# Optimization experiments

Hardware: AMD Instinct MI355X
Metric: run time of the kernel (lower is better)

Reference implementation:

```python
import jax, jax.numpy as jnp
import numpy as np

B, P, M, N, H, K, EH = 16, 50, 512, 1024, 64, 20, 200


def setup_inputs() -> dict:
    key = jax.random.key(0)
    ks = jax.random.split(key, 16)
    b = jax.random.normal(ks[0], (B, P, M, 1), jnp.float32)
    A = jax.random.normal(ks[1], (1, P, M, N), jnp.float32) / np.float32(np.sqrt(M))
    # random undirected multigraph on P nodes, stored with both directions
    s = jax.random.randint(ks[2], (B, EH), 0, P)
    off = jax.random.randint(ks[3], (B, EH), 1, P)
    d = (s + off) % P
    edge_index = jnp.stack([jnp.concatenate([s, d], 1), jnp.concatenate([d, s], 1)], 1).astype(jnp.int32)  # [B,2,2*EH]

    def lin(k, fi, fo, scale=None):
        scale = np.float32(1.0 / np.sqrt(fi)) if scale is None else np.float32(scale)
        return jax.random.normal(k, (fi, fo), jnp.float32) * scale, jnp.zeros((fo,), jnp.float32)

    W_e1, b_e1 = lin(ks[4], P * M, P * H)
    W_e2, b_e2 = lin(ks[5], P * H, 2 * P * H)
    W_e3, b_e3 = lin(ks[6], 2 * P * H, 4 * P * H)
    W_c1, b_c1 = lin(ks[7], 4 * H, 2 * H)
    W_c2, b_c2 = lin(ks[8], 2 * H, 2 * H)
    W_f1, b_f1 = lin(ks[9], 2 * H, H)
    W_f2, _ = lin(ks[10], H, K * 4, scale=1e-3)
    b_f2 = jnp.full((K * 4,), -2.0, jnp.float32)  # mimics fc2 init (tiny weights, negative bias)
    max_param = jnp.array([0.01, 0.1, 0.1, 0.1], jnp.float32).reshape(1, 1, 1, 4)  # [alpha,tau,rho,eta]_max
    y0 = jax.random.normal(ks[11], (B, P, N, 1), jnp.float32) * 0.01
    u0 = jax.random.normal(ks[12], (B, P, N, 1), jnp.float32) * 0.01
    d0 = jax.random.normal(ks[13], (B, P, N, 1), jnp.float32) * 0.01
    return dict(b=b, A=A, edge_index=edge_index, max_param=max_param,
                W_e1=W_e1, b_e1=b_e1, W_e2=W_e2, b_e2=b_e2, W_e3=W_e3, b_e3=b_e3,
                W_c1=W_c1, b_c1=b_c1, W_c2=W_c2, b_c2=b_c2,
                W_f1=W_f1, b_f1=b_f1, W_f2=W_f2, b_f2=b_f2,
                y0=y0, u0=u0, d0=d0)


def _lrelu(x):
    return jax.nn.leaky_relu(x, 0.01)


def _gcn(x, s, d, W, bias):
    # GCNConv: sym-normalized propagation with self loops. x: [P,F]
    h = x @ W
    deg = jnp.zeros((x.shape[0],), x.dtype).at[d].add(1.0) + 1.0  # +1 self loop
    dinv = jax.lax.rsqrt(deg)
    agg = jnp.zeros_like(h).at[d].add(h[s] * (dinv[s] * dinv[d])[:, None])
    agg = agg + h * (dinv * dinv)[:, None]  # self-loop term
    return agg + bias


def _delta(y, s, d):
    # nested neighbor loop: for each directed edge (s,d): delta[s]+=y[s]-y[d]; delta[d]-=same
    diff = y[s] - y[d]  # [E,N,1]
    return jnp.zeros_like(y).at[s].add(diff).at[d].add(-diff)


def reference(b, A, edge_index, max_param,
              W_e1, b_e1, W_e2, b_e2, W_e3, b_e3,
              W_c1, b_c1, W_c2, b_c2, W_f1, b_f1, W_f2, b_f2,
              y0, u0, d0):
    Bb = b.shape[0]
    n = A.shape[3]
    k_steps = W_f2.shape[1] // 4
    src, dst = edge_index[:, 0], edge_index[:, 1]

    # ---- GNN hypernetwork ----
    x = b.reshape(Bb, -1)
    x = _lrelu(x @ W_e1 + b_e1)
    x = _lrelu(x @ W_e2 + b_e2)
    x = (x @ W_e3 + b_e3).reshape(Bb, P, -1)  # [B,P,4H]
    x = _lrelu(jax.vmap(lambda xf, s, d: _gcn(xf, s, d, W_c1, b_c1))(x, src, dst))
    x = _lrelu(jax.vmap(lambda xf, s, d: _gcn(xf, s, d, W_c2, b_c2))(x, src, dst))
    x = x.mean(axis=1)  # global_mean_pool over nodes
    x = _lrelu(x @ W_f1 + b_f1)
    hyp = (x @ W_f2 + b_f2).reshape(Bb, k_steps, 1, 4)
    hyp = jax.nn.sigmoid(jnp.cumsum(hyp, axis=1)) * max_param  # [B,K,1,4]
    hyp_scan = jnp.transpose(hyp, (1, 3, 0, 2))[..., None, None]  # [K,4,B,1,1,1]

    # ---- precompute ----
    A0 = A[0]  # [P,M,N]
    AtA = jnp.einsum('pmn,pmk->pnk', A0, A0)  # [P,N,N]
    Atb = jnp.einsum('pmn,bpmo->bpno', A0, b)  # [B,P,N,1]
    sum_nb = jax.vmap(lambda s: jnp.zeros((P,), b.dtype).at[s].add(1.0))(src)[:, :, None, None]  # [B,P,1,1]

    # ---- unrolled D-ADMM / DLASSO ----
    def step(carry, hk):
        y_k, U_k, dlt = carry
        alpha, tau, rho, eta = hk[0], hk[1], hk[2], hk[3]
        AtAy = jnp.einsum('pnk,bpko->bpno', AtA, y_k)
        g = AtAy - Atb + jnp.sign(y_k) * tau + U_k * sum_nb + dlt * rho
        y_n = y_k - alpha * g
        dlt_n = jax.vmap(_delta)(y_n, src, dst)
        U_n = U_k + dlt_n * eta
        return (y_n, U_n, dlt_n), y_n

    _, Y = jax.lax.scan(step, (y0, u0, d0), hyp_scan)
    return Y  # [K,B,P,N,1]
```

## Files before the change

### kernel.cpp

```cpp
#include <hip/hip_runtime.h>

namespace {
constexpr int NB = 16;
constexpr int NP = 50;
constexpr int NM = 512;
constexpr int NN = 1024;
constexpr int NK = 20;
constexpr long ASZ = (long)NP * NM * NN;
constexpr long YSZ = (long)NB * NP * NN;
}

typedef __attribute__((ext_vector_type(8))) short bf16x8;
typedef __attribute__((ext_vector_type(4))) float f32x4;

__device__ __forceinline__ float lrelu(float x){ return x > 0.f ? x : 0.01f*x; }
__device__ __forceinline__ float bfu(unsigned short x){
  unsigned v = ((unsigned)x) << 16;
  return __builtin_bit_cast(float, v);
}
__device__ __forceinline__ unsigned short f2bf(float f){
  unsigned u = __builtin_bit_cast(unsigned, f);
  u += 0x7fffu + ((u >> 16) & 1u);
  return (unsigned short)(u >> 16);
}

__global__ __launch_bounds__(256) void k_prep(const float* __restrict__ A,
                      unsigned short* __restrict__ abfT){
  const int p = blockIdx.x, mt = blockIdx.y, nt = blockIdx.z;
  const int tid = threadIdx.x;
  __shared__ unsigned short tile[64][72];
  const int m0 = mt*64, n0 = nt*64;
  {
    int r = tid>>2, cs = (tid&3)*16;
    const float* src = A + ((long)p*NM + m0 + r)*NN + n0 + cs;
    unsigned short tmp[16];
    #pragma unroll
    for (int q=0;q<16;q+=4){
      float4 v = *(const float4*)(src+q);
      tmp[q+0]=f2bf(v.x); tmp[q+1]=f2bf(v.y); tmp[q+2]=f2bf(v.z); tmp[q+3]=f2bf(v.w);
    }
    #pragma unroll
    for (int q=0;q<16;q++) tile[r][cs+q] = tmp[q];
  }
  __syncthreads();
  {
    int r = tid>>2, cs = (tid&3)*16;
    unsigned short* dst = abfT + ((long)p*NN + n0 + r)*NM + m0 + cs;
    unsigned short tmp[16];
    #pragma unroll
    for (int q=0;q<16;q++) tmp[q] = tile[cs+q][r];
    #pragma unroll
    for (int q=0;q<16;q+=8) *(uint4*)(dst+q) = *(const uint4*)&tmp[q];
  }
}

__global__ void k_init(const float* __restrict__ y0, const float* __restrict__ u0,
                       float* __restrict__ y, float* __restrict__ u,
                       unsigned short* __restrict__ ybf, int n){
  int e = (blockIdx.x*blockDim.x + threadIdx.x)*4;
  if (e >= n) return;
  float4 a = *(const float4*)(y0+e);
  *(float4*)(y+e) = a;
  ushort4 o; o.x=f2bf(a.x); o.y=f2bf(a.y); o.z=f2bf(a.z); o.w=f2bf(a.w);
  *(ushort4*)(ybf+e) = o;
  *(float4*)(u+e)  = *(const float4*)(u0+e);
}

__global__ __launch_bounds__(256) void k_c0(const float* __restrict__ u0,
      const float* __restrict__ d0, const float* __restrict__ snbg,
      const float* __restrict__ hypg, float* __restrict__ c){
  long e = ((long)blockIdx.x*256 + threadIdx.x)*4;
  if (e >= YSZ) return;
  long bp = e >> 10;
  int b = (int)(bp/NP), p = (int)(bp%NP);
  float sp = snbg[b*NP+p], rho = hypg[b*80 + 2];
  float4 uv = *(const float4*)(u0+e);
  float4 dv = *(const float4*)(d0+e);
  float4 cv;
  cv.x = uv.x*sp + dv.x*rho; cv.y = uv.y*sp + dv.y*rho;
  cv.z = uv.z*sp + dv.z*rho; cv.w = uv.w*sp + dv.w*rho;
  *(float4*)(c+e) = cv;
}

__global__ __launch_bounds__(256) void k_atb(const unsigned short* __restrict__ abfT,
                      const float* __restrict__ src, float* __restrict__ z){
  const int p = blockIdx.x;
  const int tid = threadIdx.x, wave = tid>>6, lane = tid&63;
  __shared__ unsigned short tlds[16][520];
  {
    int b = tid>>4, c0 = (tid&15)*8;
    const float* tr = src + ((long)b*NP + p)*NM;
    #pragma unroll
    for (int it=0; it<4; it++){
      float4 lo = *(const float4*)(tr + it*128 + c0);
      float4 hi = *(const float4*)(tr + it*128 + c0 + 4);
      unsigned short w[8];
      w[0]=f2bf(lo.x); w[1]=f2bf(lo.y); w[2]=f2bf(lo.z); w[3]=f2bf(lo.w);
      w[4]=f2bf(hi.x); w[5]=f2bf(hi.y); w[6]=f2bf(hi.z); w[7]=f2bf(hi.w);
      *(uint4*)&tlds[b][it*128 + c0] = *(const uint4*)w;
    }
  }
  __syncthreads();
  const int lr = lane&15, kg = lane>>4;
  const int nt0 = blockIdx.y*4 + wave;
  const int n0 = nt0*16, n1 = (nt0+32)*16;
  const unsigned short* b0 = abfT + ((long)p*NN + n0 + lr)*NM + kg*8;
  const unsigned short* b1 = abfT + ((long)p*NN + n1 + lr)*NM + kg*8;
  const unsigned short* tp = &tlds[lr][kg*8];
  f32x4 acc0a={0.f,0.f,0.f,0.f}, acc0b={0.f,0.f,0.f,0.f};
  f32x4 acc1a={0.f,0.f,0.f,0.f}, acc1b={0.f,0.f,0.f,0.f};
  #pragma unroll 4
  for (int ks=0; ks<16; ks+=2){
    bf16x8 t0 = *(const bf16x8*)(tp + ks*32);
    bf16x8 t1 = *(const bf16x8*)(tp + ks*32 + 32);
    bf16x8 b00 = *(const bf16x8*)(b0 + (long)ks*32);
    bf16x8 b01 = *(const bf16x8*)(b0 + (long)ks*32 + 32);
    bf16x8 b10 = *(const bf16x8*)(b1 + (long)ks*32);
    bf16x8 b11 = *(const bf16x8*)(b1 + (long)ks*32 + 32);
    acc0a = __builtin_amdgcn_mfma_f32_16x16x32_bf16(t0, b00, acc0a, 0, 0, 0);
    acc1a = __builtin_amdgcn_mfma_f32_16x16x32_bf16(t0, b10, acc1a, 0, 0, 0);
    acc0b = __builtin_amdgcn_mfma_f32_16x16x32_bf16(t1, b01, acc0b, 0, 0, 0);
    acc1b = __builtin_amdgcn_mfma_f32_16x16x32_bf16(t1, b11, acc1b, 0, 0, 0);
  }
  f32x4 acc0 = acc0a + acc0b;
  f32x4 acc1 = acc1a + acc1b;
  #pragma unroll
  for (int r=0;r<4;r++){
    int bb = kg*4 + r;
    z[((long)bb*NP + p)*NN + n0 + lr] = acc0[r];
    z[((long)bb*NP + p)*NN + n1 + lr] = acc1[r];
  }
}

__global__ __launch_bounds__(256) void k_ata(const unsigned short* __restrict__ abfT,
                      unsigned short* __restrict__ ata){
  const int p = blockIdx.y;
  int yy = blockIdx.x, bi = 0;
  while (yy >= 8 - bi){ yy -= 8 - bi; bi++; }
  const int bj = bi + yy;
  const int i0 = bi*128, j0 = bj*128;
  const int tid = threadIdx.x, wave = tid>>6, lane = tid&63;
  const int lr = lane&15, kg = lane>>4;
  __shared__ unsigned short pa[128][72];
  __shared__ unsigned short pb[128][72];
  f32x4 acc[2][8];
  #pragma unroll
  for (int ti=0;ti<2;ti++)
    #pragma unroll
    for (int tj=0;tj<8;tj++) acc[ti][tj] = (f32x4){0.f,0.f,0.f,0.f};
  const unsigned short* Abase = abfT + (long)p*NN*NM;
  for (int mc=0; mc<NM; mc+=64){
    __syncthreads();
    {
      int r = tid>>1, c0 = (tid&1)*32;
      const unsigned short* sa = Abase + (long)(i0 + r)*NM + mc + c0;
      const unsigned short* sb = Abase + (long)(j0 + r)*NM + mc + c0;
      #pragma unroll
      for (int q=0;q<32;q+=8){
        *(uint4*)&pa[r][c0+q] = *(const uint4*)(sa+q);
        *(uint4*)&pb[r][c0+q] = *(const uint4*)(sb+q);
      }
    }
    __syncthreads();
    #pragma unroll
    for (int ks=0; ks<2; ks++){
      bf16x8 av0 = *(const bf16x8*)&pa[wave*32      + lr][ks*32 + kg*8];
      bf16x8 av1 = *(const bf16x8*)&pa[wave*32 + 16 + lr][ks*32 + kg*8];
      #pragma unroll
      for (int tj=0;tj<8;tj++){
        bf16x8 bv = *(const bf16x8*)&pb[tj*16 + lr][ks*32 + kg*8];
        acc[0][tj] = __builtin_amdgcn_mfma_f32_16x16x32_bf16(av0, bv, acc[0][tj], 0,0,0);
        acc[1][tj] = __builtin_amdgcn_mfma_f32_16x16x32_bf16(av1, bv, acc[1][tj], 0,0,0);
      }
    }
  }
  const long pbase = (long)p << 20;
  #pragma unroll
  for (int ti=0; ti<2; ti++){
    const int ib = i0 + wave*32 + ti*16;
    #pragma unroll
    for (int tj=0; tj<8; tj++){
      const int jb = j0 + tj*16;
      unsigned short w[4];
      #pragma unroll
      for (int r=0;r<4;r++) w[r] = f2bf(acc[ti][tj][r]);
      #pragma unroll
      for (int r=0;r<4;r++)
        ata[pbase + (long)(ib + kg*4 + r)*1024 + jb + lr] = w[r];
      if (bi != bj)
        *(ushort4*)(ata + pbase + (long)(jb + lr)*1024 + ib + kg*4) = *(const ushort4*)w;
    }
  }
}

__global__ __launch_bounds__(256) void k_enc2(const float* __restrict__ X, const float* __restrict__ W,
                           float* __restrict__ part, int fi, int fo, int ichunk, int actin){
  const int tid = threadIdx.x;
  const int o0 = (blockIdx.x*256 + tid)*4;
  const int c  = blockIdx.y;
  const bool ok = o0 < fo;
  __shared__ float xs[64][16];
  float4 acc[16];
  #pragma unroll
  for (int b=0;b<16;b++){ acc[b].x=0.f; acc[b].y=0.f; acc[b].z=0.f; acc[b].w=0.f; }
  const long ibase = (long)c*ichunk;
  const int xb = tid&15, xio = (tid>>4)*4;
  for (int s=0; s<ichunk; s+=64){
    float4 v = *(const float4*)(X + (long)xb*fi + ibase + s + xio);
    if (actin){ v.x=lrelu(v.x); v.y=lrelu(v.y); v.z=lrelu(v.z); v.w=lrelu(v.w); }
    __syncthreads();
    xs[xio+0][xb]=v.x; xs[xio+1][xb]=v.y; xs[xio+2][xb]=v.z; xs[xio+3][xb]=v.w;
    __syncthreads();
    const float* wp = W + (ibase+s)*fo + o0;
    #pragma unroll 4
    for (int i=0;i<64;i++){
      float4 w;
      if (ok) w = *(const float4*)(wp + (long)i*fo);
      else { w.x=0.f; w.y=0.f; w.z=0.f; w.w=0.f; }
      #pragma unroll
      for (int b2=0;b2<16;b2+=4){
        float4 x4 = *(const float4*)&xs[i][b2];
        acc[b2+0].x += w.x*x4.x; acc[b2+0].y += w.y*x4.x; acc[b2+0].z += w.z*x4.x; acc[b2+0].w += w.w*x4.x;
        acc[b2+1].x += w.x*x4.y; acc[b2+1].y += w.y*x4.y; acc[b2+1].z += w.z*x4.y; acc[b2+1].w += w.w*x4.y;
        acc[b2+2].x += w.x*x4.z; acc[b2+2].y += w.y*x4.z; acc[b2+2].z += w.z*x4.z; acc[b2+2].w += w.w*x4.z;
        acc[b2+3].x += w.x*x4.w; acc[b2+3].y += w.y*x4.w; acc[b2+3].z += w.z*x4.w; acc[b2+3].w += w.w*x4.w;
      }
    }
  }
  if (ok){
    float* pp = part + ((long)c*16)*fo + o0;
    #pragma unroll
    for (int b=0;b<16;b++) *(float4*)(pp + (long)b*fo) = acc[b];
  }
}

__global__ void k_enc_reduce(const float* __restrict__ part, const float* __restrict__ bias,
                             float* __restrict__ out, int fo, int nchunk){
  int i = blockIdx.x*256 + threadIdx.x;
  if (i >= 16*fo) return;
  int o = i % fo;
  float s = bias[o];
  for (int c=0;c<nchunk;c++) s += part[(long)c*16*fo + i];
  out[i] = s;
}

__global__ __launch_bounds__(64) void k_graph(const int* __restrict__ ei, float* __restrict__ adjg,
                        float* __restrict__ dmg, float* __restrict__ snbg){
  const int b = blockIdx.x, tid = threadIdx.x;
  __shared__ float adj[2500], dm[2500], deg[50], dinv[50], snb[50];
  for (int i=tid;i<2500;i+=64){ adj[i]=0.f; dm[i]=0.f; }
  if (tid<50){ deg[tid]=0.f; snb[tid]=0.f; }
  __syncthreads();
  const int* e = ei + b*800;
  for (int k=tid;k<400;k+=64){
    atomicAdd(&deg[e[400+k]], 1.f);
    atomicAdd(&snb[e[k]], 1.f);
  }
  __syncthreads();
  if (tid<50) dinv[tid] = 1.f / sqrtf(deg[tid] + 1.f);
  __syncthreads();
  for (int k=tid;k<400;k+=64){
    int s = e[k], d = e[400+k];
    atomicAdd(&adj[d*50+s], dinv[s]*dinv[d]);
    atomicAdd(&dm[s*50+s],  1.f); atomicAdd(&dm[s*50+d], -1.f);
    atomicAdd(&dm[d*50+d],  1.f); atomicAdd(&dm[d*50+s], -1.f);
  }
  __syncthreads();
  if (tid<50) adj[tid*50+tid] += dinv[tid]*dinv[tid];
  __syncthreads();
  for (int i=tid;i<2500;i+=64){ adjg[b*2500+i]=adj[i]; dmg[b*2500+i]=dm[i]; }
  if (tid<50) snbg[b*50+tid]=snb[tid];
}

__global__ __launch_bounds__(256) void k_gnn(const float* __restrict__ h3,
     const float* __restrict__ Wc1, const float* __restrict__ bc1,
     const float* __restrict__ Wc2, const float* __restrict__ bc2,
     const float* __restrict__ Wf1, const float* __restrict__ bf1,
     const float* __restrict__ Wf2, const float* __restrict__ bf2,
     const float* __restrict__ maxp, const float* __restrict__ adjg,
     float* __restrict__ hypg){
  const int b = blockIdx.x, tid = threadIdx.x;
  __shared__ float adj[2500];
  __shared__ float bufA[6400];
  __shared__ float bufB[6400];
  __shared__ float xm[128], hv1[64], raw[80];
  for (int i=tid;i<2500;i+=256) adj[i] = adjg[b*2500+i];

  const int j = tid & 127, nh = tid >> 7;
  float acc[25];
  #pragma unroll
  for (int q=0;q<25;q++) acc[q]=0.f;
  for (int ic=0; ic<4; ic++){
    __syncthreads();
    for (int e=tid; e<800; e+=256){
      int n = e>>4, seg = (e&15)*4;
      *(float4*)&bufB[n*64+seg] = *(const float4*)(h3 + (long)b*12800 + n*256 + ic*64 + seg);
    }
    __syncthreads();
    for (int i=0;i<64;i+=4){
      float w0 = Wc1[(long)(ic*64+i+0)*128 + j];
      float w1 = Wc1[(long)(ic*64+i+1)*128 + j];
      float w2 = Wc1[(long)(ic*64+i+2)*128 + j];
      float w3 = Wc1[(long)(ic*64+i+3)*128 + j];
      #pragma unroll
      for (int q=0;q<25;q++){
        float4 xv = *(const float4*)&bufB[(nh*25+q)*64 + i];
        acc[q] += xv.x*w0 + xv.y*w1 + xv.z*w2 + xv.w*w3;
      }
    }
  }
  __syncthreads();
  #pragma unroll
  for (int q=0;q<25;q++) bufA[(nh*25+q)*128 + j] = acc[q];
  __syncthreads();
  {
    float a2[25];
    float bv = bc1[j];
    #pragma unroll
    for (int q=0;q<25;q++) a2[q]=bv;
    for (int qq=0; qq<50; qq++){
      float hvv = bufA[qq*128 + j];
      #pragma unroll
      for (int q=0;q<25;q++) a2[q] += adj[(nh*25+q)*50 + qq]*hvv;
    }
    __syncthreads();
    #pragma unroll
    for (int q=0;q<25;q++) bufB[(nh*25+q)*128 + j] = lrelu(a2[q]);
  }
  __syncthreads();
  {
    float a2[25];
    #pragma unroll
    for (int q=0;q<25;q++) a2[q]=0.f;
    for (int i=0;i<128;i+=4){
      float w0 = Wc2[(long)(i+0)*128 + j];
      float w1 = Wc2[(long)(i+1)*128 + j];
      float w2 = Wc2[(long)(i+2)*128 + j];
      float w3 = Wc2[(long)(i+3)*128 + j];
      #pragma unroll
      for (int q=0;q<25;q++){
        float4 xv = *(const float4*)&bufB[(nh*25+q)*128 + i];
        a2[q] += xv.x*w0 + xv.y*w1 + xv.z*w2 + xv.w*w3;
      }
    }
    __syncthreads();
    #pragma unroll
    for (int q=0;q<25;q++) bufA[(nh*25+q)*128 + j] = a2[q];
  }
  __syncthreads();
  {
    float a2[25];
    float bv = bc2[j];
    #pragma unroll
    for (int q=0;q<25;q++) a2[q]=bv;
    for (int qq=0; qq<50; qq++){
      float hvv = bufA[qq*128 + j];
      #pragma unroll
      for (int q=0;q<25;q++) a2[q] += adj[(nh*25+q)*50 + qq]*hvv;
    }
    __syncthreads();
    #pragma unroll
    for (int q=0;q<25;q++) bufB[(nh*25+q)*128 + j] = lrelu(a2[q]);
  }
  __syncthreads();
  if (tid < 128){
    float s = 0.f;
    for (int n=0;n<50;n++) s += bufB[n*128 + tid];
    xm[tid] = s * (1.f/50.f);
  }
  __syncthreads();
  if (tid < 64){
    float s = bf1[tid];
    for (int i=0;i<128;i++) s += xm[i]*Wf1[i*64 + tid];
    hv1[tid] = lrelu(s);
  }
  __syncthreads();
  if (tid < 80){
    float s = bf2[tid];
    for (int i=0;i<64;i++) s += hv1[i]*Wf2[i*80 + tid];
    raw[tid] = s;
  }
  __syncthreads();
  if (tid < 4){
    float c = 0.f;
    for (int k=0;k<20;k++){
      c += raw[k*4 + tid];
      hypg[b*80 + k*4 + tid] = maxp[tid] / (1.f + expf(-c));
    }
  }
}

__global__ __launch_bounds__(256, 4) void k_z(const unsigned short* __restrict__ ata,
      const unsigned short* __restrict__ ybin, const float* __restrict__ atb,
      const float* __restrict__ cbuf, const float* __restrict__ hypg, int k,
      float* __restrict__ y, unsigned short* __restrict__ ybout,
      float* __restrict__ yout){
  const int p = blockIdx.x;
  const int tid = threadIdx.x, wave = tid>>6, lane = tid&63;
  __shared__ unsigned short ylds[16][1032];
  {
    int b = tid>>4, c0 = (tid&15)*8;
    const unsigned short* yr = ybin + ((long)b*NP + p)*NN;
    #pragma unroll
    for (int it=0; it<8; it++)
      *(uint4*)&ylds[b][it*128 + c0] = *(const uint4*)(yr + it*128 + c0);
  }
  const int lr = lane&15, kg = lane>>4;
  const int n0 = (blockIdx.y*4 + wave)*16;
  const long pb2 = (long)p << 20;
  const unsigned short* bp = ata + pb2 + (long)(n0 + lr)*1024 + kg*8;
  const unsigned short* yp = &ylds[lr][kg*8];

  bf16x8 B[3][4];
  #pragma unroll
  for (int j=0;j<4;j++) B[0][j] = *(const bf16x8*)(bp + (0*4+j)*32);
  #pragma unroll
  for (int j=0;j<4;j++) B[1][j] = *(const bf16x8*)(bp + (1*4+j)*32);

  float yv4[4], atb4[4], c4[4];
  float4 hp4[4];
  #pragma unroll
  for (int r=0;r<4;r++){
    const int b = kg*4 + r;
    const long idx = ((long)b*NP + p)*NN + n0 + lr;
    yv4[r] = y[idx]; atb4[r] = atb[idx]; c4[r] = cbuf[idx];
    hp4[r] = *(const float4*)(hypg + b*80 + k*4);
  }
  __syncthreads();

  f32x4 a0={0.f,0.f,0.f,0.f}, a1={0.f,0.f,0.f,0.f}, a2={0.f,0.f,0.f,0.f}, a3={0.f,0.f,0.f,0.f};
  #pragma unroll
  for (int i=0;i<8;i++){
    const int cur = i % 3;
    const int nxt = (i+2) % 3;
    if (i < 6){
      #pragma unroll
      for (int j=0;j<4;j++) B[nxt][j] = *(const bf16x8*)(bp + ((i+2)*4+j)*32);
    }
    bf16x8 q0 = *(const bf16x8*)(yp + (i*4+0)*32);
    bf16x8 q1 = *(const bf16x8*)(yp + (i*4+1)*32);
    bf16x8 q2 = *(const bf16x8*)(yp + (i*4+2)*32);
    bf16x8 q3 = *(const bf16x8*)(yp + (i*4+3)*32);
    a0 = __builtin_amdgcn_mfma_f32_16x16x32_bf16(q0, B[cur][0], a0, 0,0,0);
    a1 = __builtin_amdgcn_mfma_f32_16x16x32_bf16(q1, B[cur][1], a1, 0,0,0);
    a2 = __builtin_amdgcn_mfma_f32_16x16x32_bf16(q2, B[cur][2], a2, 0,0,0);
    a3 = __builtin_amdgcn_mfma_f32_16x16x32_bf16(q3, B[cur][3], a3, 0,0,0);
  }
  f32x4 z = (a0 + a1) + (a2 + a3);
  #pragma unroll
  for (int r=0;r<4;r++){
    const int b = kg*4 + r;
    const long idx = ((long)b*NP + p)*NN + n0 + lr;
    float yv = yv4[r];
    float g = z[r] - atb4[r] + ((yv>0.f)?1.f:((yv<0.f)?-1.f:0.f))*hp4[r].y + c4[r];
    float ynv = yv - hp4[r].x*g;
    y[idx] = ynv; ybout[idx] = f2bf(ynv); yout[(long)k*YSZ + idx] = ynv;
  }
}

__global__ __launch_bounds__(256) void k_dm(const float* __restrict__ dmg,
      const float* __restrict__ snbg, const float* __restrict__ hypg, int k,
      const unsigned short* __restrict__ ybf, float* __restrict__ u, float* __restrict__ c){
  const int b = blockIdx.x, n0 = blockIdx.y*128, tid = threadIdx.x;
  __shared__ float ys[50][128];
  __shared__ float dms[2500];
  for (int i=tid;i<2500;i+=256) dms[i] = dmg[b*2500+i];
  for (int e=tid; e<6400; e+=256){
    int p=e>>7, nn=e&127;
    ys[p][nn] = bfu(ybf[((long)b*NP+p)*NN + n0 + nn]);
  }
  __syncthreads();
  const float eta = hypg[b*80 + k*4 + 3];
  const float rhon = hypg[b*80 + (k+1)*4 + 2];
  for (int e=tid; e<6400; e+=256){
    int p=e>>7, nn=e&127;
    float s=0.f;
    #pragma unroll 10
    for (int q=0;q<NP;q++) s += dms[p*50+q]*ys[q][nn];
    long idx = ((long)b*NP+p)*NN + n0 + nn;
    float un = u[idx] + s*eta;
    u[idx] = un;
    c[idx] = un*snbg[b*NP+p] + s*rhon;
  }
}

extern "C" void kernel_launch(void* const* d_in, const int* in_sizes, int n_in,
                              void* d_out, int out_size, void* d_ws, size_t ws_size,
                              hipStream_t stream){
  (void)in_sizes; (void)n_in; (void)out_size; (void)ws_size;
  const float* bin = (const float*)d_in[0];
  const float* A   = (const float*)d_in[1];
  const int*   ei  = (const int*)d_in[2];
  const float* mxp = (const float*)d_in[3];
  const float* We1 = (const float*)d_in[4];  const float* be1 = (const float*)d_in[5];
  const float* We2 = (const float*)d_in[6];  const float* be2 = (const float*)d_in[7];
  const float* We3 = (const float*)d_in[8];  const float* be3 = (const float*)d_in[9];
  const float* Wc1 = (const float*)d_in[10]; const float* bc1 = (const float*)d_in[11];
  const float* Wc2 = (const float*)d_in[12]; const float* bc2 = (const float*)d_in[13];
  const float* Wf1 = (const float*)d_in[14]; const float* bf1 = (const float*)d_in[15];
  const float* Wf2 = (const float*)d_in[16]; const float* bf2 = (const float*)d_in[17];
  const float* y0  = (const float*)d_in[18];
  const float* u0  = (const float*)d_in[19];
  const float* dd0 = (const float*)d_in[20];
  float* out = (float*)d_out;

  char* cur = (char*)d_ws;
  auto alloc = [&](size_t bytes)->void*{
    void* pp = (void*)cur; cur += (bytes + 255) & ~(size_t)255; return pp;
  };
  unsigned short* abfT = (unsigned short*)alloc(ASZ*2);
  unsigned short* ata  = (unsigned short*)alloc((size_t)NP*1024*1024*2);
  float* atb = (float*)alloc(YSZ*4);
  float* y   = (float*)alloc(YSZ*4);
  unsigned short* ybf0 = (unsigned short*)alloc(YSZ*2);
  unsigned short* ybf1 = (unsigned short*)alloc(YSZ*2);
  float* u   = (float*)alloc(YSZ*4);
  float* cb  = (float*)alloc(YSZ*4);
  float* h1  = (float*)alloc((size_t)16*3200*4);
  float* h2  = (float*)alloc((size_t)16*6400*4);
  float* h3  = (float*)alloc((size_t)16*12800*4);
  float* adj = (float*)alloc((size_t)16*2500*4);
  float* dm  = (float*)alloc((size_t)16*2500*4);
  float* snb = (float*)alloc((size_t)16*50*4);
  float* hyp = (float*)alloc((size_t)16*80*4);
  float* part= (float*)alloc((size_t)84000000);

  k_prep<<<dim3(50,8,16), dim3(256), 0, stream>>>(A, abfT);
  k_init<<<dim3(800), dim3(256), 0, stream>>>(y0, u0, y, u, ybf0, (int)YSZ);
  k_atb<<<dim3(50,8), dim3(256), 0, stream>>>(abfT, bin, atb);
  k_ata<<<dim3(36,50), dim3(256), 0, stream>>>(abfT, ata);

  k_enc2<<<dim3(4,200),  dim3(256), 0, stream>>>(bin, We1, part, 25600, 3200, 128, 0);
  k_enc_reduce<<<dim3(200), dim3(256), 0, stream>>>(part, be1, h1, 3200, 200);
  k_enc2<<<dim3(7,50),  dim3(256), 0, stream>>>(h1, We2, part, 3200, 6400, 64, 1);
  k_enc_reduce<<<dim3(400), dim3(256), 0, stream>>>(part, be2, h2, 6400, 50);
  k_enc2<<<dim3(13,100), dim3(256), 0, stream>>>(h2, We3, part, 6400, 12800, 64, 1);
  k_enc_reduce<<<dim3(800), dim3(256), 0, stream>>>(part, be3, h3, 12800, 100);

  k_graph<<<dim3(16), dim3(64), 0, stream>>>(ei, adj, dm, snb);
  k_gnn<<<dim3(16), dim3(256), 0, stream>>>(h3, Wc1, bc1, Wc2, bc2, Wf1, bf1, Wf2, bf2, mxp, adj, hyp);
  k_c0<<<dim3(800), dim3(256), 0, stream>>>(u0, dd0, snb, hyp, cb);

  for (int k=0;k<NK;k++){
    const unsigned short* ybin = (k & 1) ? ybf1 : ybf0;
    unsigned short* ybout      = (k & 1) ? ybf0 : ybf1;
    k_z<<<dim3(50,16), dim3(256), 0, stream>>>(ata, ybin, atb, cb, hyp, k, y, ybout, out);
    if (k < NK-1){
      const unsigned short* ybnew = (k & 1) ? ybf0 : ybf1;
      k_dm<<<dim3(16,8), dim3(256), 0, stream>>>(dm, snb, hyp, k, ybnew, u, cb);
    }
  }
}
```

Before: 1.532 ms.

## Tile AtA layout for contiguous MFMA loads and fold Atb into state buffer

Stores AtA in a 16x32 tiled layout so each wave's B-fragment loads in k_z read contiguous 512-element tiles instead of rows strided by 1024 elements. It also replaces the U state with w = U*sum_nb - Atb and precomputes e = w + rho*delta, so k_z reads one fp32 buffer per element instead of two. The tiled layout makes k_ata's transposed writes scalar and scattered, and the algebraic fold changes float rounding order slightly.

Result: faster. 1.485 ms (-3.0%).

```diff
diff --git a/kernel.cpp b/kernel.cpp
--- a/kernel.cpp
+++ b/kernel.cpp
@@ -23,6 +23,9 @@
   u += 0x7fffu + ((u >> 16) & 1u);
   return (unsigned short)(u >> 16);
 }
+__device__ __forceinline__ long toff(int n, int kk){
+  return (long)(n>>4)*16384 + (long)(kk>>5)*512 + (long)((n&15)*32 + ((kk>>3)&3)*8 + (kk&7));
+}
 
 __global__ __launch_bounds__(256) void k_prep(const float* __restrict__ A,
                       unsigned short* __restrict__ abfT){
@@ -54,8 +57,7 @@
   }
 }
 
-__global__ void k_init(const float* __restrict__ y0, const float* __restrict__ u0,
-                       float* __restrict__ y, float* __restrict__ u,
+__global__ void k_init(const float* __restrict__ y0, float* __restrict__ y,
                        unsigned short* __restrict__ ybf, int n){
   int e = (blockIdx.x*blockDim.x + threadIdx.x)*4;
   if (e >= n) return;
@@ -63,23 +65,27 @@
   *(float4*)(y+e) = a;
   ushort4 o; o.x=f2bf(a.x); o.y=f2bf(a.y); o.z=f2bf(a.z); o.w=f2bf(a.w);
   *(ushort4*)(ybf+e) = o;
-  *(float4*)(u+e)  = *(const float4*)(u0+e);
-}
-
-__global__ __launch_bounds__(256) void k_c0(const float* __restrict__ u0,
-      const float* __restrict__ d0, const float* __restrict__ snbg,
-      const float* __restrict__ hypg, float* __restrict__ c){
-  long e = ((long)blockIdx.x*256 + threadIdx.x)*4;
-  if (e >= YSZ) return;
-  long bp = e >> 10;
+}
+
+__global__ __launch_bounds__(256) void k_e0(const float* __restrict__ u0,
+      const float* __restrict__ d0, const float* __restrict__ atb,
+      const float* __restrict__ snbg, const float* __restrict__ hypg,
+      float* __restrict__ w, float* __restrict__ e){
+  long i = ((long)blockIdx.x*256 + threadIdx.x)*4;
+  if (i >= YSZ) return;
+  long bp = i >> 10;
   int b = (int)(bp/NP), p = (int)(bp%NP);
   float sp = snbg[b*NP+p], rho = hypg[b*80 + 2];
-  float4 uv = *(const float4*)(u0+e);
-  float4 dv = *(const float4*)(d0+e);
-  float4 cv;
-  cv.x = uv.x*sp + dv.x*rho; cv.y = uv.y*sp + dv.y*rho;
-  cv.z = uv.z*sp + dv.z*rho; cv.w = uv.w*sp + dv.w*rho;
-  *(float4*)(c+e) = cv;
+  float4 uv = *(const float4*)(u0+i);
+  float4 dv = *(const float4*)(d0+i);
+  float4 av = *(const float4*)(atb+i);
+  float4 wv, ev;
+  wv.x = uv.x*sp - av.x; wv.y = uv.y*sp - av.y;
+  wv.z = uv.z*sp - av.z; wv.w = uv.w*sp - av.w;
+  ev.x = wv.x + dv.x*rho; ev.y = wv.y + dv.y*rho;
+  ev.z = wv.z + dv.z*rho; ev.w = wv.w + dv.w*rho;
+  *(float4*)(w+i) = wv;
+  *(float4*)(e+i) = ev;
 }
 
 __global__ __launch_bounds__(256) void k_atb(const unsigned short* __restrict__ abfT,
@@ -186,9 +192,12 @@
       for (int r=0;r<4;r++) w[r] = f2bf(acc[ti][tj][r]);
       #pragma unroll
       for (int r=0;r<4;r++)
-        ata[pbase + (long)(ib + kg*4 + r)*1024 + jb + lr] = w[r];
-      if (bi != bj)
-        *(ushort4*)(ata + pbase + (long)(jb + lr)*1024 + ib + kg*4) = *(const ushort4*)w;
+        ata[pbase + toff(ib + kg*4 + r, jb + lr)] = w[r];
+      if (bi != bj){
+        #pragma unroll
+        for (int r=0;r<4;r++)
+          ata[pbase + toff(jb + lr, ib + kg*4 + r)] = w[r];
+      }
     }
   }
 }
@@ -391,8 +400,8 @@
 }
 
 __global__ __launch_bounds__(256, 4) void k_z(const unsigned short* __restrict__ ata,
-      const unsigned short* __restrict__ ybin, const float* __restrict__ atb,
-      const float* __restrict__ cbuf, const float* __restrict__ hypg, int k,
+      const unsigned short* __restrict__ ybin, const float* __restrict__ ebuf,
+      const float* __restrict__ hypg, int k,
       float* __restrict__ y, unsigned short* __restrict__ ybout,
       float* __restrict__ yout){
   const int p = blockIdx.x;
@@ -406,24 +415,24 @@
       *(uint4*)&ylds[b][it*128 + c0] = *(const uint4*)(yr + it*128 + c0);
   }
   const int lr = lane&15, kg = lane>>4;
-  const int n0 = (blockIdx.y*4 + wave)*16;
-  const long pb2 = (long)p << 20;
-  const unsigned short* bp = ata + pb2 + (long)(n0 + lr)*1024 + kg*8;
+  const int t  = blockIdx.y*4 + wave;
+  const int n0 = t*16;
+  const unsigned short* bp = ata + ((long)p<<20) + (long)t*16384 + lr*32 + kg*8;
   const unsigned short* yp = &ylds[lr][kg*8];
 
   bf16x8 B[3][4];
   #pragma unroll
-  for (int j=0;j<4;j++) B[0][j] = *(const bf16x8*)(bp + (0*4+j)*32);
-  #pragma unroll
-  for (int j=0;j<4;j++) B[1][j] = *(const bf16x8*)(bp + (1*4+j)*32);
-
-  float yv4[4], atb4[4], c4[4];
+  for (int j=0;j<4;j++) B[0][j] = *(const bf16x8*)(bp + (0*4+j)*512);
+  #pragma unroll
+  for (int j=0;j<4;j++) B[1][j] = *(const bf16x8*)(bp + (1*4+j)*512);
+
+  float yv4[4], e4[4];
   float4 hp4[4];
   #pragma unroll
   for (int r=0;r<4;r++){
     const int b = kg*4 + r;
     const long idx = ((long)b*NP + p)*NN + n0 + lr;
-    yv4[r] = y[idx]; atb4[r] = atb[idx]; c4[r] = cbuf[idx];
+    yv4[r] = y[idx]; e4[r] = ebuf[idx];
     hp4[r] = *(const float4*)(hypg + b*80 + k*4);
   }
   __syncthreads();
@@ -435,7 +444,7 @@
     const int nxt = (i+2) % 3;
     if (i < 6){
       #pragma unroll
-      for (int j=0;j<4;j++) B[nxt][j] = *(const bf16x8*)(bp + ((i+2)*4+j)*32);
+      for (int j=0;j<4;j++) B[nxt][j] = *(const bf16x8*)(bp + ((i+2)*4+j)*512);
     }
     bf16x8 q0 = *(const bf16x8*)(yp + (i*4+0)*32);
     bf16x8 q1 = *(const bf16x8*)(yp + (i*4+1)*32);
@@ -452,7 +461,7 @@
     const int b = kg*4 + r;
     const long idx = ((long)b*NP + p)*NN + n0 + lr;
     float yv = yv4[r];
-    float g = z[r] - atb4[r] + ((yv>0.f)?1.f:((yv<0.f)?-1.f:0.f))*hp4[r].y + c4[r];
+    float g = z[r] + ((yv>0.f)?1.f:((yv<0.f)?-1.f:0.f))*hp4[r].y + e4[r];
     float ynv = yv - hp4[r].x*g;
     y[idx] = ynv; ybout[idx] = f2bf(ynv); yout[(long)k*YSZ + idx] = ynv;
   }
@@ -460,27 +469,27 @@
 
 __global__ __launch_bounds__(256) void k_dm(const float* __restrict__ dmg,
       const float* __restrict__ snbg, const float* __restrict__ hypg, int k,
-      const unsigned short* __restrict__ ybf, float* __restrict__ u, float* __restrict__ c){
+      const unsigned short* __restrict__ ybf, float* __restrict__ w, float* __restrict__ e){
   const int b = blockIdx.x, n0 = blockIdx.y*128, tid = threadIdx.x;
   __shared__ float ys[50][128];
   __shared__ float dms[2500];
   for (int i=tid;i<2500;i+=256) dms[i] = dmg[b*2500+i];
-  for (int e=tid; e<6400; e+=256){
-    int p=e>>7, nn=e&127;
+  for (int i=tid; i<6400; i+=256){
+    int p=i>>7, nn=i&127;
     ys[p][nn] = bfu(ybf[((long)b*NP+p)*NN + n0 + nn]);
   }
   __syncthreads();
   const float eta = hypg[b*80 + k*4 + 3];
   const float rhon = hypg[b*80 + (k+1)*4 + 2];
-  for (int e=tid; e<6400; e+=256){
-    int p=e>>7, nn=e&127;
+  for (int i=tid; i<6400; i+=256){
+    int p=i>>7, nn=i&127;
     float s=0.f;
     #pragma unroll 10
     for (int q=0;q<NP;q++) s += dms[p*50+q]*ys[q][nn];
     long idx = ((long)b*NP+p)*NN + n0 + nn;
-    float un = u[idx] + s*eta;
-    u[idx] = un;
-    c[idx] = un*snbg[b*NP+p] + s*rhon;
+    float wn = w[idx] + s*eta*snbg[b*NP+p];
+    w[idx] = wn;
+    e[idx] = wn + s*rhon;
   }
 }
 
@@ -514,8 +523,8 @@
   float* y   = (float*)alloc(YSZ*4);
   unsigned short* ybf0 = (unsigned short*)alloc(YSZ*2);
   unsigned short* ybf1 = (unsigned short*)alloc(YSZ*2);
-  float* u   = (float*)alloc(YSZ*4);
-  float* cb  = (float*)alloc(YSZ*4);
+  float* w   = (float*)alloc(YSZ*4);
+  float* eb  = (float*)alloc(YSZ*4);
   float* h1  = (float*)alloc((size_t)16*3200*4);
   float* h2  = (float*)alloc((size_t)16*6400*4);
   float* h3  = (float*)alloc((size_t)16*12800*4);
@@ -526,7 +535,7 @@
   float* part= (float*)alloc((size_t)84000000);
 
   k_prep<<<dim3(50,8,16), dim3(256), 0, stream>>>(A, abfT);
-  k_init<<<dim3(800), dim3(256), 0, stream>>>(y0, u0, y, u, ybf0, (int)YSZ);
+  k_init<<<dim3(800), dim3(256), 0, stream>>>(y0, y, ybf0, (int)YSZ);
   k_atb<<<dim3(50,8), dim3(256), 0, stream>>>(abfT, bin, atb);
   k_ata<<<dim3(36,50), dim3(256), 0, stream>>>(abfT, ata);
 
@@ -539,15 +548,15 @@
 
   k_graph<<<dim3(16), dim3(64), 0, stream>>>(ei, adj, dm, snb);
   k_gnn<<<dim3(16), dim3(256), 0, stream>>>(h3, Wc1, bc1, Wc2, bc2, Wf1, bf1, Wf2, bf2, mxp, adj, hyp);
-  k_c0<<<dim3(800), dim3(256), 0, stream>>>(u0, dd0, snb, hyp, cb);
+  k_e0<<<dim3(800), dim3(256), 0, stream>>>(u0, dd0, atb, snb, hyp, w, eb);
 
   for (int k=0;k<NK;k++){
     const unsigned short* ybin = (k & 1) ? ybf1 : ybf0;
     unsigned short* ybout      = (k & 1) ? ybf0 : ybf1;
-    k_z<<<dim3(50,16), dim3(256), 0, stream>>>(ata, ybin, atb, cb, hyp, k, y, ybout, out);
+    k_z<<<dim3(50,16), dim3(256), 0, stream>>>(ata, ybin, eb, hyp, k, y, ybout, out);
     if (k < NK-1){
       const unsigned short* ybnew = (k & 1) ? ybf0 : ybf1;
-      k_dm<<<dim3(16,8), dim3(256), 0, stream>>>(dm, snb, hyp, k, ybnew, u, cb);
-    }
-  }
-}
+      k_dm<<<dim3(16,8), dim3(256), 0, stream>>>(dm, snb, hyp, k, ybnew, w, eb);
+    }
+  }
+}
```
